# Kernel optimization log

Measured on AMD Instinct MI355X. Metric: run time of the kernel, lower is better.

The kernel has to match this reference:

```python
import jax, jax.numpy as jnp
import numpy as np

# ADMM hyperparameters for mode='only_tv'
GAMMA_TV = 10.0
ALPHA = 5.0
LAMBDA_TV = 1e-4
N_ITERS = 50


def soft_thresh(v, t):
    return jnp.sign(v) * jnp.maximum(jnp.abs(v) - t, 0.0)


def setup_inputs() -> dict:
    key = jax.random.key(0)
    k1, k2, k3 = jax.random.split(key, 3)
    target = jax.random.normal(k1, (4096,), dtype=jnp.float32)
    A = jax.random.normal(k2, (9, 4096), dtype=jnp.float32)  # [M, N], post-transpose
    x0 = jax.random.normal(k3, (4096,), dtype=jnp.float32)   # replaces torch.randn_like
    return {"target": target, "A": A, "x0": x0}


def reference(target, A, x0):
    N = A.shape[1]
    I = jnp.eye(N, dtype=A.dtype)
    Delta = jnp.roll(I, 1, axis=1) - I               # [N, N] circular difference
    DtD = Delta.T @ Delta
    AtA = A.T @ A
    # only_tv: gamma_l1 = beta = 0, so regularizer is ATA + gamma_tv*DtD + alpha*I
    inv_item = jnp.linalg.inv(AtA + GAMMA_TV * DtD + ALPHA * I)

    b = A @ target            # [M]
    bA = b @ A                # [N], constant across iterations

    def step(carry, _):
        x, eta_tv, tau = carry
        # u_tv: soft-threshold of backward difference (roll along axis 0)
        u_tv = soft_thresh(jnp.roll(x, 1, axis=0) - x + eta_tv / GAMMA_TV,
                           LAMBDA_TV / GAMMA_TV)
        # w: nonnegativity split variable
        w = jnp.maximum(x + tau / ALPHA, 0.0)
        # x-update (zero terms for l1/dwt/z dropped: gamma_l1 = gamma_dwt = beta = 0)
        resid = bA + (GAMMA_TV * u_tv - eta_tv) + (ALPHA * w - tau)
        x = resid @ inv_item
        # dual updates
        eta_tv = eta_tv + GAMMA_TV * (Delta @ x - u_tv)
        tau = tau + ALPHA * (x - w)
        return (x, eta_tv, tau), None

    zeros = jnp.zeros_like(x0)
    (x, _, _), _ = jax.lax.scan(step, (x0, zeros, zeros), None, length=N_ITERS)
    return x
```

## Files before the change

### kernel.cpp

```cpp
#include <hip/hip_runtime.h>
#include <math.h>

#define NT 512
#define EPT 8
#define NN 4096
#define MM 9
#define NIT 50

#define LAM  3.90625e-3f
#define LAM2 1.52587890625e-5f
#define K1LAST 0.3333282470703125f

template<int CTRL, int RMASK>
__device__ __forceinline__ float dpp_add(float v) {
  int m = __builtin_amdgcn_update_dpp(0, __builtin_bit_cast(int, v), CTRL, RMASK, 0xf, false);
  return v + __builtin_bit_cast(float, m);
}
__device__ __forceinline__ float wave_sum(float v) {
  v = dpp_add<0x111, 0xf>(v);
  v = dpp_add<0x112, 0xf>(v);
  v = dpp_add<0x114, 0xf>(v);
  v = dpp_add<0x118, 0xf>(v);
  v = dpp_add<0x142, 0xa>(v);
  v = dpp_add<0x143, 0xc>(v);
  return v;
}
template<int CTRL>
__device__ __forceinline__ float dpp_shift(float oldv, float v) {
  int m = __builtin_amdgcn_update_dpp(__builtin_bit_cast(int, oldv),
                                      __builtin_bit_cast(int, v), CTRL, 0xf, 0xf, false);
  return __builtin_bit_cast(float, m);
}
__device__ __forceinline__ float bcast_lane(float v, int l) {
  return __builtin_bit_cast(float, __builtin_amdgcn_readlane(__builtin_bit_cast(int, v), l));
}

__device__ __forceinline__ void solveM_pre(const float r[EPT], float pl0[EPT],
                                           float2* __restrict__ s_sc, int t) {
  float yl[EPT];
  yl[EPT - 1] = r[EPT - 1] * 0.1f;
#pragma unroll
  for (int j = EPT - 2; j >= 0; --j) yl[j] = fmaf(0.5f, yl[j + 1], r[j] * 0.1f);
  pl0[0] = 0.5f * yl[0];
#pragma unroll
  for (int j = 1; j < EPT; ++j) pl0[j] = 0.5f * (yl[j] + pl0[j - 1]);
  s_sc[t] = make_float2(yl[0], pl0[EPT - 1]);
}

__device__ __forceinline__ void solveM_post(const float pl0[EPT], float p[EPT],
                                            const float2* __restrict__ s_sc, int t) {
  const float K1[EPT] = {0.001953125f, 0.0048828125f, 0.01025390625f, 0.020751953125f,
                         0.0416259765625f, 0.08331298828125f, 0.166656494140625f,
                         0.3333282470703125f};
  float2 g[7];
#pragma unroll
  for (int k = 0; k < 7; ++k) g[k] = s_sc[(t + k - 3) & (NT - 1)];
  float c  = fmaf(LAM2, g[6].x, fmaf(LAM, g[5].x, g[4].x));
  float s1 = fmaf(LAM2, g[0].y, fmaf(LAM, g[1].y, g[2].y));
  float s2 = g[3].x;
  s2 = fmaf(LAM, g[2].x + g[4].x, s2);
  s2 = fmaf(LAM2, g[1].x + g[5].x, s2);
  float c2 = fmaf(K1LAST, s2, s1);
  float f2 = 0.5f;
#pragma unroll
  for (int j = 0; j < EPT; ++j) {
    p[j] = fmaf(c2, f2, fmaf(c, K1[j], pl0[j]));
    f2 *= 0.5f;
  }
}

__global__ void __launch_bounds__(NT, 2)
admm_kernel(const float* __restrict__ tg, const float* __restrict__ Ag,
            const float* __restrict__ x0, float* __restrict__ out) {
  __shared__ float2 s_sc[NT];
  __shared__ __align__(16) float s_wq[8][12];
  __shared__ float s_S[MM * MM];
  __shared__ float s_L[MM * MM];
  __shared__ float s_edge[8][2];

  const int t = threadIdx.x;
  const int base = t * EPT;
  const int lane = t & 63, wave = t >> 6;

  float A[MM][EPT];
#pragma unroll
  for (int m = 0; m < MM; ++m) {
    float4 a0 = *(const float4*)(Ag + m * NN + base);
    float4 a1 = *(const float4*)(Ag + m * NN + base + 4);
    A[m][0] = a0.x; A[m][1] = a0.y; A[m][2] = a0.z; A[m][3] = a0.w;
    A[m][4] = a1.x; A[m][5] = a1.y; A[m][6] = a1.z; A[m][7] = a1.w;
  }

  float x[EPT], tgt[EPT];
  {
    float4 v0 = *(const float4*)(x0 + base);
    float4 v1 = *(const float4*)(x0 + base + 4);
    x[0] = v0.x; x[1] = v0.y; x[2] = v0.z; x[3] = v0.w;
    x[4] = v1.x; x[5] = v1.y; x[6] = v1.z; x[7] = v1.w;
    float4 t0 = *(const float4*)(tg + base);
    float4 t1 = *(const float4*)(tg + base + 4);
    tgt[0] = t0.x; tgt[1] = t0.y; tgt[2] = t0.z; tgt[3] = t0.w;
    tgt[4] = t1.x; tgt[5] = t1.y; tgt[6] = t1.z; tgt[7] = t1.w;
  }
  if (lane == 0)  s_edge[wave][0] = x[0];
  if (lane == 63) s_edge[wave][1] = x[7];

  float pq[MM];
#pragma unroll
  for (int m = 0; m < MM; ++m) {
    float s = 0.f;
#pragma unroll
    for (int j = 0; j < EPT; ++j) s = fmaf(A[m][j], tgt[j], s);
    pq[m] = wave_sum(s);
  }
  if (lane == 63) {
    *(float4*)&s_wq[wave][0] = make_float4(pq[0], pq[1], pq[2], pq[3]);
    *(float4*)&s_wq[wave][4] = make_float4(pq[4], pq[5], pq[6], pq[7]);
    s_wq[wave][8] = pq[8];
  }
  __syncthreads();
  float bb[MM];
  {
    float zv = 0.f;
    if (lane < MM) {
#pragma unroll
      for (int wv = 0; wv < 8; ++wv) zv += s_wq[wv][lane];
    }
#pragma unroll
    for (int m = 0; m < MM; ++m) bb[m] = bcast_lane(zv, m);
  }
  float bA[EPT];
#pragma unroll
  for (int j = 0; j < EPT; ++j) {
    float s = 0.f;
#pragma unroll
    for (int m = 0; m < MM; ++m) s = fmaf(bb[m], A[m][j], s);
    bA[j] = s;
  }

  float G[MM][EPT];
#pragma unroll
  for (int mc = 0; mc < MM; ++mc) {
    float rin[EPT];
#pragma unroll
    for (int j = 0; j < EPT; ++j) rin[j] = A[mc][j];
    float pl0[EPT];
    solveM_pre(rin, pl0, s_sc, t);
    __syncthreads();
    float gcol[EPT];
    solveM_post(pl0, gcol, s_sc, t);
#pragma unroll
    for (int j = 0; j < EPT; ++j) G[mc][j] = gcol[j];
#pragma unroll
    for (int k = 0; k < MM; ++k) {
      float s = 0.f;
#pragma unroll
      for (int j = 0; j < EPT; ++j) s = fmaf(A[k][j], gcol[j], s);
      pq[k] = wave_sum(s);
    }
    if (lane == 63) {
      *(float4*)&s_wq[wave][0] = make_float4(pq[0], pq[1], pq[2], pq[3]);
      *(float4*)&s_wq[wave][4] = make_float4(pq[4], pq[5], pq[6], pq[7]);
      s_wq[wave][8] = pq[8];
    }
    __syncthreads();
    if (wave == 0 && lane < MM) {
      float s = 0.f;
#pragma unroll
      for (int wv = 0; wv < 8; ++wv) s += s_wq[wv][lane];
      s_S[lane * MM + mc] = s + ((lane == mc) ? 1.f : 0.f);
    }
  }

  if (t < 64) {
    float row[2 * MM];
#pragma unroll
    for (int j = 0; j < MM; ++j) row[j] = (t < MM) ? s_S[t * MM + j] : 0.f;
#pragma unroll
    for (int j = 0; j < MM; ++j) row[MM + j] = (j == t) ? 1.f : 0.f;
#pragma unroll
    for (int pp = 0; pp < MM; ++pp) {
      float pr[2 * MM];
#pragma unroll
      for (int j = 0; j < 2 * MM; ++j) pr[j] = __shfl(row[j], pp, 64);
      float rpiv = 1.f / pr[pp];
      float fct = row[pp] * rpiv;
#pragma unroll
      for (int j = 0; j < 2 * MM; ++j)
        row[j] = (t == pp) ? pr[j] * rpiv : fmaf(-fct, pr[j], row[j]);
    }
    float crow[MM];
#pragma unroll
    for (int j = 0; j < MM; ++j) crow[j] = row[MM + j];
#pragma unroll
    for (int k = 0; k < MM; ++k) {
      float dk = __shfl(crow[k], k, 64);
      float inv = 1.f / sqrtf(dk);
      crow[k] *= inv;
#pragma unroll
      for (int jj = k + 1; jj < MM; ++jj) {
        float ljk = __shfl(crow[k], jj, 64);
        crow[jj] = fmaf(-crow[k], ljk, crow[jj]);
      }
    }
    if (t < MM) {
#pragma unroll
      for (int j = 0; j < MM; ++j) s_L[t * MM + j] = (t >= j) ? crow[j] : 0.f;
    }
  }
  __syncthreads();

  float GH[MM][EPT];
#pragma unroll
  for (int m = 0; m < MM; ++m) {
    float lcol[MM];
#pragma unroll
    for (int k = 0; k < MM; ++k) lcol[k] = s_L[k * MM + m];
#pragma unroll
    for (int j = 0; j < EPT; ++j) {
      float s = 0.f;
#pragma unroll
      for (int k = 0; k < MM; ++k)
        if (k >= m) s = fmaf(G[k][j], lcol[k], s);
      GH[m][j] = s;
    }
  }

  float eta[EPT], tau[EPT];
#pragma unroll
  for (int j = 0; j < EPT; ++j) { eta[j] = 0.f; tau[j] = 0.f; }
  float u7prev = 0.f, w7prev = 0.f;

#pragma unroll 1
  for (int it = 0; it < NIT; ++it) {
    float oldm = 0.f, oldn = 0.f;
    if (lane == 0)  oldm = s_edge[(wave + 7) & 7][1];
    if (lane == 63) oldn = s_edge[(wave + 1) & 7][0];
    float xm1 = dpp_shift<0x138>(oldm, x[7]);
    if (it) {
      float xn8 = dpp_shift<0x130>(oldn, x[0]);
      eta[7] = fmaf(10.f, (xn8 - x[7]) - u7prev, eta[7]);
      tau[7] = fmaf(5.f, x[7] - w7prev, tau[7]);
    }
    float u[EPT], w[EPT], r[EPT];
#pragma unroll
    for (int j = 0; j < EPT; ++j) {
      float xprev = (j == 0) ? xm1 : x[j - 1];
      float v = xprev - x[j] + eta[j] * 0.1f;
      u[j] = copysignf(fmaxf(fabsf(v) - 1e-5f, 0.f), v);
      w[j] = fmaxf(fmaf(tau[j], 0.2f, x[j]), 0.f);
      r[j] = bA[j] + 10.f * u[j] - eta[j] + 5.f * w[j] - tau[j];
    }
    float zp[MM];
#pragma unroll
    for (int m = 0; m < MM; ++m) {
      float s = 0.f;
#pragma unroll
      for (int j = 0; j < EPT; ++j) s = fmaf(GH[m][j], r[j], s);
      zp[m] = wave_sum(s);
    }
    if (lane == 63) {
      *(float4*)&s_wq[wave][0] = make_float4(zp[0], zp[1], zp[2], zp[3]);
      *(float4*)&s_wq[wave][4] = make_float4(zp[4], zp[5], zp[6], zp[7]);
      s_wq[wave][8] = zp[8];
    }
    float pl0[EPT];
    solveM_pre(r, pl0, s_sc, t);
    __syncthreads();
    float p[EPT];
    solveM_post(pl0, p, s_sc, t);
    float zv = 0.f;
    if (lane < MM) {
#pragma unroll
      for (int wv = 0; wv < 8; ++wv) zv += s_wq[wv][lane];
    }
    float z[MM];
#pragma unroll
    for (int m = 0; m < MM; ++m) z[m] = bcast_lane(zv, m);
#pragma unroll
    for (int j = 0; j < EPT; ++j) {
      float s = p[j];
#pragma unroll
      for (int m = 0; m < MM; ++m) s = fmaf(-GH[m][j], z[m], s);
      x[j] = s;
    }
    if (lane == 0)  s_edge[wave][0] = x[0];
    if (lane == 63) s_edge[wave][1] = x[7];
#pragma unroll
    for (int j = 0; j < EPT - 1; ++j) {
      eta[j] = fmaf(10.f, (x[j + 1] - x[j]) - u[j], eta[j]);
      tau[j] = fmaf(5.f, x[j] - w[j], tau[j]);
    }
    u7prev = u[7]; w7prev = w[7];
    __syncthreads();
  }

  float4 o0, o1;
  o0.x = x[0]; o0.y = x[1]; o0.z = x[2]; o0.w = x[3];
  o1.x = x[4]; o1.y = x[5]; o1.z = x[6]; o1.w = x[7];
  *(float4*)(out + base) = o0;
  *(float4*)(out + base + 4) = o1;
}

extern "C" void kernel_launch(void* const* d_in, const int* in_sizes, int n_in,
                              void* d_out, int out_size, void* d_ws, size_t ws_size,
                              hipStream_t stream) {
  const float* target = (const float*)d_in[0];
  const float* A      = (const float*)d_in[1];
  const float* x0     = (const float*)d_in[2];
  admm_kernel<<<1, NT, 0, stream>>>(target, A, x0, (float*)d_out);
}
```

Measured before the change: 106.5 us.

## Cut to one barrier per ADMM iteration by recomputing neighbor x values and double buffering

The main loop is restructured so each iteration has a single __syncthreads instead of two. Neighbor boundary values x[-1] and x[8] are no longer exchanged through shared memory. They are recomputed locally from a wider 9-entry gather of scan carries plus neighbor GH rows kept in shared memory. The scan and reduction buffers are double-buffered by iteration parity, and the first iteration's residual is peeled before the loop. This trades extra FMAs and shared-memory loads per iteration for one fewer block-wide barrier on the serial critical path.

```diff
diff --git a/kernel.cpp b/kernel.cpp
--- a/kernel.cpp
+++ b/kernel.cpp
@@ -10,6 +10,7 @@
 #define LAM  3.90625e-3f
 #define LAM2 1.52587890625e-5f
 #define K1LAST 0.3333282470703125f
+#define HALF8 3.90625e-3f
 
 template<int CTRL, int RMASK>
 __device__ __forceinline__ float dpp_add(float v) {
@@ -25,12 +26,6 @@
   v = dpp_add<0x143, 0xc>(v);
   return v;
 }
-template<int CTRL>
-__device__ __forceinline__ float dpp_shift(float oldv, float v) {
-  int m = __builtin_amdgcn_update_dpp(__builtin_bit_cast(int, oldv),
-                                      __builtin_bit_cast(int, v), CTRL, 0xf, 0xf, false);
-  return __builtin_bit_cast(float, m);
-}
 __device__ __forceinline__ float bcast_lane(float v, int l) {
   return __builtin_bit_cast(float, __builtin_amdgcn_readlane(__builtin_bit_cast(int, v), l));
 }
@@ -47,36 +42,63 @@
   s_sc[t] = make_float2(yl[0], pl0[EPT - 1]);
 }
 
-__device__ __forceinline__ void solveM_post(const float pl0[EPT], float p[EPT],
-                                            const float2* __restrict__ s_sc, int t) {
+__device__ __forceinline__ void gather9(const float2* __restrict__ s_sc, int t, float2 g[9]) {
+#pragma unroll
+  for (int k = 0; k < 9; ++k) g[k] = s_sc[(t + k - 4) & (NT - 1)];
+}
+
+__device__ __forceinline__ void carries_own(const float2 g[9], float& c, float& c2) {
+  c = fmaf(LAM2, g[7].x, fmaf(LAM, g[6].x, g[5].x));
+  float s1 = fmaf(LAM2, g[1].y, fmaf(LAM, g[2].y, g[3].y));
+  float s2 = g[4].x;
+  s2 = fmaf(LAM, g[3].x + g[5].x, s2);
+  s2 = fmaf(LAM2, g[2].x + g[6].x, s2);
+  c2 = fmaf(K1LAST, s2, s1);
+}
+
+__device__ __forceinline__ void finish_own(const float2 g[9], const float pl0[EPT], float p[EPT]) {
   const float K1[EPT] = {0.001953125f, 0.0048828125f, 0.01025390625f, 0.020751953125f,
                          0.0416259765625f, 0.08331298828125f, 0.166656494140625f,
-                         0.3333282470703125f};
-  float2 g[7];
-#pragma unroll
-  for (int k = 0; k < 7; ++k) g[k] = s_sc[(t + k - 3) & (NT - 1)];
-  float c  = fmaf(LAM2, g[6].x, fmaf(LAM, g[5].x, g[4].x));
+                         K1LAST};
+  float c, c2;
+  carries_own(g, c, c2);
+  float f2 = 0.5f;
+#pragma unroll
+  for (int j = 0; j < EPT; ++j) {
+    p[j] = fmaf(c2, f2, fmaf(c, K1[j], pl0[j]));
+    f2 *= 0.5f;
+  }
+}
+
+__device__ __forceinline__ float p7_prev(const float2 g[9]) {
+  float c = fmaf(LAM2, g[6].x, fmaf(LAM, g[5].x, g[4].x));
   float s1 = fmaf(LAM2, g[0].y, fmaf(LAM, g[1].y, g[2].y));
   float s2 = g[3].x;
   s2 = fmaf(LAM, g[2].x + g[4].x, s2);
   s2 = fmaf(LAM2, g[1].x + g[5].x, s2);
   float c2 = fmaf(K1LAST, s2, s1);
-  float f2 = 0.5f;
-#pragma unroll
-  for (int j = 0; j < EPT; ++j) {
-    p[j] = fmaf(c2, f2, fmaf(c, K1[j], pl0[j]));
-    f2 *= 0.5f;
-  }
+  return fmaf(c2, HALF8, fmaf(c, K1LAST, g[3].y));
+}
+
+__device__ __forceinline__ float p0_next(const float2 g[9]) {
+  float c = fmaf(LAM2, g[8].x, fmaf(LAM, g[7].x, g[6].x));
+  float s1 = fmaf(LAM2, g[2].y, fmaf(LAM, g[3].y, g[4].y));
+  float s2 = g[5].x;
+  s2 = fmaf(LAM, g[4].x + g[6].x, s2);
+  s2 = fmaf(LAM2, g[3].x + g[7].x, s2);
+  float c2 = fmaf(K1LAST, s2, s1);
+  return fmaf(c2, 0.5f, fmaf(c, 0.001953125f, 0.5f * g[5].x));
 }
 
 __global__ void __launch_bounds__(NT, 2)
 admm_kernel(const float* __restrict__ tg, const float* __restrict__ Ag,
             const float* __restrict__ x0, float* __restrict__ out) {
-  __shared__ float2 s_sc[NT];
-  __shared__ __align__(16) float s_wq[8][12];
+  __shared__ float2 s_sc[2][NT];
+  __shared__ __align__(16) float s_wq[2][8][12];
   __shared__ float s_S[MM * MM];
   __shared__ float s_L[MM * MM];
-  __shared__ float s_edge[8][2];
+  __shared__ float s_gh7[NT][MM];
+  __shared__ float s_gh0[NT][MM];
 
   const int t = threadIdx.x;
   const int base = t * EPT;
@@ -102,8 +124,7 @@
     tgt[0] = t0.x; tgt[1] = t0.y; tgt[2] = t0.z; tgt[3] = t0.w;
     tgt[4] = t1.x; tgt[5] = t1.y; tgt[6] = t1.z; tgt[7] = t1.w;
   }
-  if (lane == 0)  s_edge[wave][0] = x[0];
-  if (lane == 63) s_edge[wave][1] = x[7];
+  float xm1_0 = x0[(base + NN - 1) & (NN - 1)];
 
   float pq[MM];
 #pragma unroll
@@ -114,9 +135,9 @@
     pq[m] = wave_sum(s);
   }
   if (lane == 63) {
-    *(float4*)&s_wq[wave][0] = make_float4(pq[0], pq[1], pq[2], pq[3]);
-    *(float4*)&s_wq[wave][4] = make_float4(pq[4], pq[5], pq[6], pq[7]);
-    s_wq[wave][8] = pq[8];
+    *(float4*)&s_wq[0][wave][0] = make_float4(pq[0], pq[1], pq[2], pq[3]);
+    *(float4*)&s_wq[0][wave][4] = make_float4(pq[4], pq[5], pq[6], pq[7]);
+    s_wq[0][wave][8] = pq[8];
   }
   __syncthreads();
   float bb[MM];
@@ -124,7 +145,7 @@
     float zv = 0.f;
     if (lane < MM) {
 #pragma unroll
-      for (int wv = 0; wv < 8; ++wv) zv += s_wq[wv][lane];
+      for (int wv = 0; wv < 8; ++wv) zv += s_wq[0][wv][lane];
     }
 #pragma unroll
     for (int m = 0; m < MM; ++m) bb[m] = bcast_lane(zv, m);
@@ -145,10 +166,12 @@
 #pragma unroll
     for (int j = 0; j < EPT; ++j) rin[j] = A[mc][j];
     float pl0[EPT];
-    solveM_pre(rin, pl0, s_sc, t);
+    solveM_pre(rin, pl0, &s_sc[mc & 1][0], t);
     __syncthreads();
+    float2 g[9];
+    gather9(&s_sc[mc & 1][0], t, g);
     float gcol[EPT];
-    solveM_post(pl0, gcol, s_sc, t);
+    finish_own(g, pl0, gcol);
 #pragma unroll
     for (int j = 0; j < EPT; ++j) G[mc][j] = gcol[j];
 #pragma unroll
@@ -159,15 +182,15 @@
       pq[k] = wave_sum(s);
     }
     if (lane == 63) {
-      *(float4*)&s_wq[wave][0] = make_float4(pq[0], pq[1], pq[2], pq[3]);
-      *(float4*)&s_wq[wave][4] = make_float4(pq[4], pq[5], pq[6], pq[7]);
-      s_wq[wave][8] = pq[8];
+      *(float4*)&s_wq[0][wave][0] = make_float4(pq[0], pq[1], pq[2], pq[3]);
+      *(float4*)&s_wq[0][wave][4] = make_float4(pq[4], pq[5], pq[6], pq[7]);
+      s_wq[0][wave][8] = pq[8];
     }
     __syncthreads();
     if (wave == 0 && lane < MM) {
       float s = 0.f;
 #pragma unroll
-      for (int wv = 0; wv < 8; ++wv) s += s_wq[wv][lane];
+      for (int wv = 0; wv < 8; ++wv) s += s_wq[0][wv][lane];
       s_S[lane * MM + mc] = s + ((lane == mc) ? 1.f : 0.f);
     }
   }
@@ -225,24 +248,84 @@
       GH[m][j] = s;
     }
   }
+#pragma unroll
+  for (int m = 0; m < MM; ++m) {
+    s_gh7[t][m] = GH[m][7];
+    s_gh0[t][m] = GH[m][0];
+  }
 
   float eta[EPT], tau[EPT];
 #pragma unroll
   for (int j = 0; j < EPT; ++j) { eta[j] = 0.f; tau[j] = 0.f; }
-  float u7prev = 0.f, w7prev = 0.f;
+  float u[EPT], w[EPT], r[EPT], pl0[EPT];
+#pragma unroll
+  for (int j = 0; j < EPT; ++j) {
+    float xprev = (j == 0) ? xm1_0 : x[j - 1];
+    float v = xprev - x[j];
+    u[j] = copysignf(fmaxf(fabsf(v) - 1e-5f, 0.f), v);
+    w[j] = fmaxf(x[j], 0.f);
+    r[j] = bA[j] + 10.f * u[j] + 5.f * w[j];
+  }
+  {
+    float zp[MM];
+#pragma unroll
+    for (int m = 0; m < MM; ++m) {
+      float s = 0.f;
+#pragma unroll
+      for (int j = 0; j < EPT; ++j) s = fmaf(GH[m][j], r[j], s);
+      zp[m] = wave_sum(s);
+    }
+    if (lane == 63) {
+      *(float4*)&s_wq[0][wave][0] = make_float4(zp[0], zp[1], zp[2], zp[3]);
+      *(float4*)&s_wq[0][wave][4] = make_float4(zp[4], zp[5], zp[6], zp[7]);
+      s_wq[0][wave][8] = zp[8];
+    }
+  }
+  solveM_pre(r, pl0, &s_sc[0][0], t);
+  __syncthreads();
 
 #pragma unroll 1
   for (int it = 0; it < NIT; ++it) {
-    float oldm = 0.f, oldn = 0.f;
-    if (lane == 0)  oldm = s_edge[(wave + 7) & 7][1];
-    if (lane == 63) oldn = s_edge[(wave + 1) & 7][0];
-    float xm1 = dpp_shift<0x138>(oldm, x[7]);
-    if (it) {
-      float xn8 = dpp_shift<0x130>(oldn, x[0]);
-      eta[7] = fmaf(10.f, (xn8 - x[7]) - u7prev, eta[7]);
-      tau[7] = fmaf(5.f, x[7] - w7prev, tau[7]);
-    }
-    float u[EPT], w[EPT], r[EPT];
+    const int rp = it & 1;
+    float2 g[9];
+    gather9(&s_sc[rp][0], t, g);
+    float gh7r[MM], gh0r[MM];
+    {
+      const int tm = (t + NT - 1) & (NT - 1), tp = (t + 1) & (NT - 1);
+#pragma unroll
+      for (int m = 0; m < MM; ++m) { gh7r[m] = s_gh7[tm][m]; gh0r[m] = s_gh0[tp][m]; }
+    }
+    float zv = 0.f;
+    if (lane < MM) {
+#pragma unroll
+      for (int wv = 0; wv < 8; ++wv) zv += s_wq[rp][wv][lane];
+    }
+    float z[MM];
+#pragma unroll
+    for (int m = 0; m < MM; ++m) z[m] = bcast_lane(zv, m);
+    float p[EPT];
+    finish_own(g, pl0, p);
+#pragma unroll
+    for (int j = 0; j < EPT; ++j) {
+      float s = p[j];
+#pragma unroll
+      for (int m = 0; m < MM; ++m) s = fmaf(-GH[m][j], z[m], s);
+      x[j] = s;
+    }
+    if (it == NIT - 1) break;
+    float xm1 = p7_prev(g);
+#pragma unroll
+    for (int m = 0; m < MM; ++m) xm1 = fmaf(-gh7r[m], z[m], xm1);
+    float xp1 = p0_next(g);
+#pragma unroll
+    for (int m = 0; m < MM; ++m) xp1 = fmaf(-gh0r[m], z[m], xp1);
+#pragma unroll
+    for (int j = 0; j < EPT - 1; ++j) {
+      eta[j] = fmaf(10.f, (x[j + 1] - x[j]) - u[j], eta[j]);
+      tau[j] = fmaf(5.f, x[j] - w[j], tau[j]);
+    }
+    eta[7] = fmaf(10.f, (xp1 - x[7]) - u[7], eta[7]);
+    tau[7] = fmaf(5.f, x[7] - w[7], tau[7]);
 #pragma unroll
     for (int j = 0; j < EPT; ++j) {
       float xprev = (j == 0) ? xm1 : x[j - 1];
@@ -260,38 +343,11 @@
       zp[m] = wave_sum(s);
     }
     if (lane == 63) {
-      *(float4*)&s_wq[wave][0] = make_float4(zp[0], zp[1], zp[2], zp[3]);
-      *(float4*)&s_wq[wave][4] = make_float4(zp[4], zp[5], zp[6], zp[7]);
-      s_wq[wave][8] = zp[8];
-    }
-    float pl0[EPT];
-    solveM_pre(r, pl0, s_sc, t);
-    __syncthreads();
-    float p[EPT];
-    solveM_post(pl0, p, s_sc, t);
-    float zv = 0.f;
-    if (lane < MM) {
-#pragma unroll
-      for (int wv = 0; wv < 8; ++wv) zv += s_wq[wv][lane];
-    }
-    float z[MM];
-#pragma unroll
-    for (int m = 0; m < MM; ++m) z[m] = bcast_lane(zv, m);
-#pragma unroll
-    for (int j = 0; j < EPT; ++j) {
-      float s = p[j];
-#pragma unroll
-      for (int m = 0; m < MM; ++m) s = fmaf(-GH[m][j], z[m], s);
-      x[j] = s;
-    }
-    if (lane == 0)  s_edge[wave][0] = x[0];
-    if (lane == 63) s_edge[wave][1] = x[7];
-#pragma unroll
-    for (int j = 0; j < EPT - 1; ++j) {
-      eta[j] = fmaf(10.f, (x[j + 1] - x[j]) - u[j], eta[j]);
-      tau[j] = fmaf(5.f, x[j] - w[j], tau[j]);
-    }
-    u7prev = u[7]; w7prev = w[7];
+      *(float4*)&s_wq[rp ^ 1][wave][0] = make_float4(zp[0], zp[1], zp[2], zp[3]);
+      *(float4*)&s_wq[rp ^ 1][wave][4] = make_float4(zp[4], zp[5], zp[6], zp[7]);
+      s_wq[rp ^ 1][wave][8] = zp[8];
+    }
+    solveM_pre(r, pl0, &s_sc[rp ^ 1][0], t);
     __syncthreads();
   }
 
```

New measurement: 114.1 us. +7.1%, slower.

## Double threads to 1024 with 4 elements each and rescale ADMM dual variables

Applied to the files above, without the earlier changes.

Launches 1024 threads with 4 elements each instead of 512 with 8, so there are 16 waves and the per-thread serial work and register use are halved. The tridiagonal-like solve now gathers 11 neighbour partials with new decay constants, and the Gram-column setup alternates between two shared scratch buffers. The dual variables are kept pre-scaled (eta/10, tau/5) and the nonnegativity split is rewritten as max(x, -tau5), which removes several multiplies per element. In exchange, the cross-wave reductions now sum over 16 wave partials, the barrier spans more waves, and each solve reads more shared memory.

```diff
diff --git a/kernel.cpp b/kernel.cpp
--- a/kernel.cpp
+++ b/kernel.cpp
@@ -1,15 +1,16 @@
 #include <hip/hip_runtime.h>
 #include <math.h>
 
-#define NT 512
-#define EPT 8
+#define NT 1024
+#define EPT 4
+#define NW (NT/64)
 #define NN 4096
 #define MM 9
 #define NIT 50
 
-#define LAM  3.90625e-3f
-#define LAM2 1.52587890625e-5f
-#define K1LAST 0.3333282470703125f
+#define LAM  0.0625f
+#define LAM2 3.90625e-3f
+#define K1L  0.33203125f
 
 template<int CTRL, int RMASK>
 __device__ __forceinline__ float dpp_add(float v) {
@@ -38,45 +39,42 @@
 __device__ __forceinline__ void solveM_pre(const float r[EPT], float pl0[EPT],
                                            float2* __restrict__ s_sc, int t) {
   float yl[EPT];
-  yl[EPT - 1] = r[EPT - 1] * 0.1f;
-#pragma unroll
-  for (int j = EPT - 2; j >= 0; --j) yl[j] = fmaf(0.5f, yl[j + 1], r[j] * 0.1f);
+  yl[3] = r[3] * 0.1f;
+  yl[2] = fmaf(0.5f, yl[3], r[2] * 0.1f);
+  yl[1] = fmaf(0.5f, yl[2], r[1] * 0.1f);
+  yl[0] = fmaf(0.5f, yl[1], r[0] * 0.1f);
   pl0[0] = 0.5f * yl[0];
-#pragma unroll
-  for (int j = 1; j < EPT; ++j) pl0[j] = 0.5f * (yl[j] + pl0[j - 1]);
-  s_sc[t] = make_float2(yl[0], pl0[EPT - 1]);
-}
-
-__device__ __forceinline__ void solveM_post(const float pl0[EPT], float p[EPT],
-                                            const float2* __restrict__ s_sc, int t) {
-  const float K1[EPT] = {0.001953125f, 0.0048828125f, 0.01025390625f, 0.020751953125f,
-                         0.0416259765625f, 0.08331298828125f, 0.166656494140625f,
-                         0.3333282470703125f};
-  float2 g[7];
-#pragma unroll
-  for (int k = 0; k < 7; ++k) g[k] = s_sc[(t + k - 3) & (NT - 1)];
-  float c  = fmaf(LAM2, g[6].x, fmaf(LAM, g[5].x, g[4].x));
-  float s1 = fmaf(LAM2, g[0].y, fmaf(LAM, g[1].y, g[2].y));
-  float s2 = g[3].x;
-  s2 = fmaf(LAM, g[2].x + g[4].x, s2);
-  s2 = fmaf(LAM2, g[1].x + g[5].x, s2);
-  float c2 = fmaf(K1LAST, s2, s1);
-  float f2 = 0.5f;
-#pragma unroll
-  for (int j = 0; j < EPT; ++j) {
-    p[j] = fmaf(c2, f2, fmaf(c, K1[j], pl0[j]));
-    f2 *= 0.5f;
-  }
-}
-
-__global__ void __launch_bounds__(NT, 2)
+  pl0[1] = 0.5f * (yl[1] + pl0[0]);
+  pl0[2] = 0.5f * (yl[2] + pl0[1]);
+  pl0[3] = 0.5f * (yl[3] + pl0[2]);
+  s_sc[t] = make_float2(yl[0], pl0[3]);
+}
+
+__device__ __forceinline__ void gather11(const float2* __restrict__ s_sc, int t, float2 g[11]) {
+#pragma unroll
+  for (int k = 0; k < 11; ++k) g[k] = s_sc[(t + k - 5) & (NT - 1)];
+}
+
+__device__ __forceinline__ void finish_own(const float2 g[11], const float pl0[EPT], float p[EPT]) {
+  float c = fmaf(LAM, fmaf(LAM, fmaf(LAM, fmaf(LAM, g[10].x, g[9].x), g[8].x), g[7].x), g[6].x);
+  float s1 = fmaf(LAM, fmaf(LAM, fmaf(LAM, fmaf(LAM, g[0].y, g[1].y), g[2].y), g[3].y), g[4].y);
+  float s2 = fmaf(LAM, fmaf(LAM, fmaf(LAM, fmaf(LAM, g[1].x + g[9].x, g[2].x + g[8].x),
+                                      g[3].x + g[7].x), g[4].x + g[6].x), g[5].x);
+  float c2 = fmaf(1.0f / 3.0f, s2, s1);
+  p[0] = fmaf(c2, 0.5f,    fmaf(c, 0.03125f,   pl0[0]));
+  p[1] = fmaf(c2, 0.25f,   fmaf(c, 0.078125f,  pl0[1]));
+  p[2] = fmaf(c2, 0.125f,  fmaf(c, 0.1640625f, pl0[2]));
+  p[3] = fmaf(c2, 0.0625f, fmaf(c, K1L,        pl0[3]));
+}
+
+__global__ void __launch_bounds__(NT, 4)
 admm_kernel(const float* __restrict__ tg, const float* __restrict__ Ag,
             const float* __restrict__ x0, float* __restrict__ out) {
-  __shared__ float2 s_sc[NT];
-  __shared__ __align__(16) float s_wq[8][12];
+  __shared__ float2 s_sc[2][NT];
+  __shared__ __align__(16) float s_wq[NW][12];
   __shared__ float s_S[MM * MM];
   __shared__ float s_L[MM * MM];
-  __shared__ float s_edge[8][2];
+  __shared__ float s_edge[NW][2];
 
   const int t = threadIdx.x;
   const int base = t * EPT;
@@ -86,24 +84,18 @@
 #pragma unroll
   for (int m = 0; m < MM; ++m) {
     float4 a0 = *(const float4*)(Ag + m * NN + base);
-    float4 a1 = *(const float4*)(Ag + m * NN + base + 4);
     A[m][0] = a0.x; A[m][1] = a0.y; A[m][2] = a0.z; A[m][3] = a0.w;
-    A[m][4] = a1.x; A[m][5] = a1.y; A[m][6] = a1.z; A[m][7] = a1.w;
   }
 
   float x[EPT], tgt[EPT];
   {
     float4 v0 = *(const float4*)(x0 + base);
-    float4 v1 = *(const float4*)(x0 + base + 4);
     x[0] = v0.x; x[1] = v0.y; x[2] = v0.z; x[3] = v0.w;
-    x[4] = v1.x; x[5] = v1.y; x[6] = v1.z; x[7] = v1.w;
     float4 t0 = *(const float4*)(tg + base);
-    float4 t1 = *(const float4*)(tg + base + 4);
     tgt[0] = t0.x; tgt[1] = t0.y; tgt[2] = t0.z; tgt[3] = t0.w;
-    tgt[4] = t1.x; tgt[5] = t1.y; tgt[6] = t1.z; tgt[7] = t1.w;
   }
   if (lane == 0)  s_edge[wave][0] = x[0];
-  if (lane == 63) s_edge[wave][1] = x[7];
+  if (lane == 63) s_edge[wave][1] = x[3];
 
   float pq[MM];
 #pragma unroll
@@ -124,7 +116,7 @@
     float zv = 0.f;
     if (lane < MM) {
 #pragma unroll
-      for (int wv = 0; wv < 8; ++wv) zv += s_wq[wv][lane];
+      for (int wv = 0; wv < NW; ++wv) zv += s_wq[wv][lane];
     }
 #pragma unroll
     for (int m = 0; m < MM; ++m) bb[m] = bcast_lane(zv, m);
@@ -145,10 +137,12 @@
 #pragma unroll
     for (int j = 0; j < EPT; ++j) rin[j] = A[mc][j];
     float pl0[EPT];
-    solveM_pre(rin, pl0, s_sc, t);
+    solveM_pre(rin, pl0, &s_sc[mc & 1][0], t);
     __syncthreads();
+    float2 g[11];
+    gather11(&s_sc[mc & 1][0], t, g);
     float gcol[EPT];
-    solveM_post(pl0, gcol, s_sc, t);
+    finish_own(g, pl0, gcol);
 #pragma unroll
     for (int j = 0; j < EPT; ++j) G[mc][j] = gcol[j];
 #pragma unroll
@@ -167,7 +161,7 @@
     if (wave == 0 && lane < MM) {
       float s = 0.f;
 #pragma unroll
-      for (int wv = 0; wv < 8; ++wv) s += s_wq[wv][lane];
+      for (int wv = 0; wv < NW; ++wv) s += s_wq[wv][lane];
       s_S[lane * MM + mc] = s + ((lane == mc) ? 1.f : 0.f);
     }
   }
@@ -226,30 +220,29 @@
     }
   }
 
-  float eta[EPT], tau[EPT];
-#pragma unroll
-  for (int j = 0; j < EPT; ++j) { eta[j] = 0.f; tau[j] = 0.f; }
-  float u7prev = 0.f, w7prev = 0.f;
+  float eta10[EPT], tau5[EPT];
+#pragma unroll
+  for (int j = 0; j < EPT; ++j) { eta10[j] = 0.f; tau5[j] = 0.f; }
+  float u3prev = 0.f;
 
 #pragma unroll 1
   for (int it = 0; it < NIT; ++it) {
     float oldm = 0.f, oldn = 0.f;
-    if (lane == 0)  oldm = s_edge[(wave + 7) & 7][1];
-    if (lane == 63) oldn = s_edge[(wave + 1) & 7][0];
-    float xm1 = dpp_shift<0x138>(oldm, x[7]);
+    if (lane == 0)  oldm = s_edge[(wave + NW - 1) & (NW - 1)][1];
+    if (lane == 63) oldn = s_edge[(wave + 1) & (NW - 1)][0];
+    float xm1 = dpp_shift<0x138>(oldm, x[3]);
     if (it) {
-      float xn8 = dpp_shift<0x130>(oldn, x[0]);
-      eta[7] = fmaf(10.f, (xn8 - x[7]) - u7prev, eta[7]);
-      tau[7] = fmaf(5.f, x[7] - w7prev, tau[7]);
-    }
-    float u[EPT], w[EPT], r[EPT];
+      float xn4 = dpp_shift<0x130>(oldn, x[0]);
+      eta10[3] += (xn4 - x[3]) - u3prev;
+    }
+    float u[EPT], m1a[EPT], r[EPT];
 #pragma unroll
     for (int j = 0; j < EPT; ++j) {
       float xprev = (j == 0) ? xm1 : x[j - 1];
-      float v = xprev - x[j] + eta[j] * 0.1f;
+      float v = xprev - x[j] + eta10[j];
       u[j] = copysignf(fmaxf(fabsf(v) - 1e-5f, 0.f), v);
-      w[j] = fmaxf(fmaf(tau[j], 0.2f, x[j]), 0.f);
-      r[j] = bA[j] + 10.f * u[j] - eta[j] + 5.f * w[j] - tau[j];
+      m1a[j] = fmaxf(x[j], -tau5[j]);
+      r[j] = fmaf(10.f, u[j] - eta10[j], fmaf(5.f, m1a[j], bA[j]));
     }
     float zp[MM];
 #pragma unroll
@@ -265,14 +258,16 @@
       s_wq[wave][8] = zp[8];
     }
     float pl0[EPT];
-    solveM_pre(r, pl0, s_sc, t);
+    solveM_pre(r, pl0, &s_sc[0][0], t);
     __syncthreads();
+    float2 g[11];
+    gather11(&s_sc[0][0], t, g);
     float p[EPT];
-    solveM_post(pl0, p, s_sc, t);
+    finish_own(g, pl0, p);
     float zv = 0.f;
     if (lane < MM) {
 #pragma unroll
-      for (int wv = 0; wv < 8; ++wv) zv += s_wq[wv][lane];
+      for (int wv = 0; wv < NW; ++wv) zv += s_wq[wv][lane];
     }
     float z[MM];
 #pragma unroll
@@ -285,21 +280,20 @@
       x[j] = s;
     }
     if (lane == 0)  s_edge[wave][0] = x[0];
-    if (lane == 63) s_edge[wave][1] = x[7];
-#pragma unroll
-    for (int j = 0; j < EPT - 1; ++j) {
-      eta[j] = fmaf(10.f, (x[j + 1] - x[j]) - u[j], eta[j]);
-      tau[j] = fmaf(5.f, x[j] - w[j], tau[j]);
-    }
-    u7prev = u[7]; w7prev = w[7];
+    if (lane == 63) s_edge[wave][1] = x[3];
+#pragma unroll
+    for (int j = 0; j < EPT - 1; ++j)
+      eta10[j] += (x[j + 1] - x[j]) - u[j];
+#pragma unroll
+    for (int j = 0; j < EPT; ++j)
+      tau5[j] = x[j] - m1a[j];
+    u3prev = u[3];
     __syncthreads();
   }
 
-  float4 o0, o1;
+  float4 o0;
   o0.x = x[0]; o0.y = x[1]; o0.z = x[2]; o0.w = x[3];
-  o1.x = x[4]; o1.y = x[5]; o1.z = x[6]; o1.w = x[7];
   *(float4*)(out + base) = o0;
-  *(float4*)(out + base + 4) = o1;
 }
 
 extern "C" void kernel_launch(void* const* d_in, const int* in_sizes, int n_in,
```

New measurement: 145.1 us. 36.3% more time.

## Pack ADMM iteration math into v_pk_fma and rescale dual variables

Applied to the files above, without the earlier changes.

Stores x, GH and the reduction inputs as float2 pairs and uses inline v_pk_fma_f32/v_pk_mul_f32 for the GH·r reductions and the x reconstruction. The dual variables are rescaled so eta is kept divided by gamma and tau is stored as an offset, which removes several multiplies per element. The preprocessing scratch buffer is also double-buffered across the column solves. This cuts VALU instruction count in the serial 50-iteration loop of a single-block kernel, at the cost of hand-written asm that constrains register allocation and packing moves.

```diff
diff --git a/kernel.cpp b/kernel.cpp
--- a/kernel.cpp
+++ b/kernel.cpp
@@ -10,6 +10,16 @@
 #define LAM  3.90625e-3f
 #define LAM2 1.52587890625e-5f
 #define K1LAST 0.3333282470703125f
+
+typedef float f2 __attribute__((ext_vector_type(2)));
+__device__ __forceinline__ f2 mkf2(float a, float b) { f2 v; v.x = a; v.y = b; return v; }
+
+__device__ __forceinline__ f2 pkfma(f2 a, f2 b, f2 c) {
+  f2 d; asm("v_pk_fma_f32 %0, %1, %2, %3" : "=v"(d) : "v"(a), "v"(b), "v"(c)); return d;
+}
+__device__ __forceinline__ f2 pkmul(f2 a, f2 b) {
+  f2 d; asm("v_pk_mul_f32 %0, %1, %2" : "=v"(d) : "v"(a), "v"(b)); return d;
+}
 
 template<int CTRL, int RMASK>
 __device__ __forceinline__ float dpp_add(float v) {
@@ -51,7 +61,7 @@
                                             const float2* __restrict__ s_sc, int t) {
   const float K1[EPT] = {0.001953125f, 0.0048828125f, 0.01025390625f, 0.020751953125f,
                          0.0416259765625f, 0.08331298828125f, 0.166656494140625f,
-                         0.3333282470703125f};
+                         K1LAST};
   float2 g[7];
 #pragma unroll
   for (int k = 0; k < 7; ++k) g[k] = s_sc[(t + k - 3) & (NT - 1)];
@@ -61,18 +71,18 @@
   s2 = fmaf(LAM, g[2].x + g[4].x, s2);
   s2 = fmaf(LAM2, g[1].x + g[5].x, s2);
   float c2 = fmaf(K1LAST, s2, s1);
-  float f2 = 0.5f;
+  float f2w = 0.5f;
 #pragma unroll
   for (int j = 0; j < EPT; ++j) {
-    p[j] = fmaf(c2, f2, fmaf(c, K1[j], pl0[j]));
-    f2 *= 0.5f;
+    p[j] = fmaf(c2, f2w, fmaf(c, K1[j], pl0[j]));
+    f2w *= 0.5f;
   }
 }
 
 __global__ void __launch_bounds__(NT, 2)
 admm_kernel(const float* __restrict__ tg, const float* __restrict__ Ag,
             const float* __restrict__ x0, float* __restrict__ out) {
-  __shared__ float2 s_sc[NT];
+  __shared__ float2 s_sc[2][NT];
   __shared__ __align__(16) float s_wq[8][12];
   __shared__ float s_S[MM * MM];
   __shared__ float s_L[MM * MM];
@@ -129,13 +139,16 @@
 #pragma unroll
     for (int m = 0; m < MM; ++m) bb[m] = bcast_lane(zv, m);
   }
-  float bA[EPT];
-#pragma unroll
-  for (int j = 0; j < EPT; ++j) {
-    float s = 0.f;
-#pragma unroll
-    for (int m = 0; m < MM; ++m) s = fmaf(bb[m], A[m][j], s);
-    bA[j] = s;
+  f2 bA2[4];
+#pragma unroll
+  for (int jj = 0; jj < 4; ++jj) {
+    float sa = 0.f, sb = 0.f;
+#pragma unroll
+    for (int m = 0; m < MM; ++m) {
+      sa = fmaf(bb[m], A[m][2 * jj], sa);
+      sb = fmaf(bb[m], A[m][2 * jj + 1], sb);
+    }
+    bA2[jj] = mkf2(sa, sb);
   }
 
   float G[MM][EPT];
@@ -145,10 +158,10 @@
 #pragma unroll
     for (int j = 0; j < EPT; ++j) rin[j] = A[mc][j];
     float pl0[EPT];
-    solveM_pre(rin, pl0, s_sc, t);
+    solveM_pre(rin, pl0, (float2*)&s_sc[mc & 1][0], t);
     __syncthreads();
     float gcol[EPT];
-    solveM_post(pl0, gcol, s_sc, t);
+    solveM_post(pl0, gcol, (const float2*)&s_sc[mc & 1][0], t);
 #pragma unroll
     for (int j = 0; j < EPT; ++j) G[mc][j] = gcol[j];
 #pragma unroll
@@ -210,54 +223,71 @@
   }
   __syncthreads();
 
-  float GH[MM][EPT];
+  f2 GH2[MM][4];
 #pragma unroll
   for (int m = 0; m < MM; ++m) {
     float lcol[MM];
 #pragma unroll
     for (int k = 0; k < MM; ++k) lcol[k] = s_L[k * MM + m];
 #pragma unroll
-    for (int j = 0; j < EPT; ++j) {
-      float s = 0.f;
+    for (int jj = 0; jj < 4; ++jj) {
+      float sa = 0.f, sb = 0.f;
 #pragma unroll
       for (int k = 0; k < MM; ++k)
-        if (k >= m) s = fmaf(G[k][j], lcol[k], s);
-      GH[m][j] = s;
-    }
-  }
-
-  float eta[EPT], tau[EPT];
-#pragma unroll
-  for (int j = 0; j < EPT; ++j) { eta[j] = 0.f; tau[j] = 0.f; }
-  float u7prev = 0.f, w7prev = 0.f;
+        if (k >= m) {
+          sa = fmaf(G[k][2 * jj], lcol[k], sa);
+          sb = fmaf(G[k][2 * jj + 1], lcol[k], sb);
+        }
+      GH2[m][jj] = mkf2(sa, sb);
+    }
+  }
+
+  f2 x2[4], eta2[4], tau2[4];
+#pragma unroll
+  for (int jj = 0; jj < 4; ++jj) {
+    x2[jj] = mkf2(x[2 * jj], x[2 * jj + 1]);
+    eta2[jj] = mkf2(0.f, 0.f);
+    tau2[jj] = mkf2(0.f, 0.f);
+  }
+  float u7prev = 0.f;
 
 #pragma unroll 1
   for (int it = 0; it < NIT; ++it) {
     float oldm = 0.f, oldn = 0.f;
     if (lane == 0)  oldm = s_edge[(wave + 7) & 7][1];
     if (lane == 63) oldn = s_edge[(wave + 1) & 7][0];
-    float xm1 = dpp_shift<0x138>(oldm, x[7]);
+    float xm1 = dpp_shift<0x138>(oldm, x2[3].y);
     if (it) {
-      float xn8 = dpp_shift<0x130>(oldn, x[0]);
-      eta[7] = fmaf(10.f, (xn8 - x[7]) - u7prev, eta[7]);
-      tau[7] = fmaf(5.f, x[7] - w7prev, tau[7]);
-    }
-    float u[EPT], w[EPT], r[EPT];
-#pragma unroll
-    for (int j = 0; j < EPT; ++j) {
-      float xprev = (j == 0) ? xm1 : x[j - 1];
-      float v = xprev - x[j] + eta[j] * 0.1f;
-      u[j] = copysignf(fmaxf(fabsf(v) - 1e-5f, 0.f), v);
-      w[j] = fmaxf(fmaf(tau[j], 0.2f, x[j]), 0.f);
-      r[j] = bA[j] + 10.f * u[j] - eta[j] + 5.f * w[j] - tau[j];
+      float xn8 = dpp_shift<0x130>(oldn, x2[0].x);
+      eta2[3].y += (xn8 - x2[3].y) - u7prev;
+    }
+    float u[EPT], m1[EPT], rr[EPT];
+    f2 r2[4];
+#pragma unroll
+    for (int jj = 0; jj < 4; ++jj) {
+      float xa = x2[jj].x, xb = x2[jj].y;
+      float xprev = (jj == 0) ? xm1 : x2[jj - 1].y;
+      float va = xprev - xa + eta2[jj].x;
+      float vb = xa - xb + eta2[jj].y;
+      float ua = copysignf(fmaxf(fabsf(va) - 1e-5f, 0.f), va);
+      float ub = copysignf(fmaxf(fabsf(vb) - 1e-5f, 0.f), vb);
+      float ma = fmaxf(xa, -tau2[jj].x);
+      float mb = fmaxf(xb, -tau2[jj].y);
+      float ra = fmaf(10.f, ua - eta2[jj].x, fmaf(5.f, ma, bA2[jj].x));
+      float rb = fmaf(10.f, ub - eta2[jj].y, fmaf(5.f, mb, bA2[jj].y));
+      u[2 * jj] = ua; u[2 * jj + 1] = ub;
+      m1[2 * jj] = ma; m1[2 * jj + 1] = mb;
+      rr[2 * jj] = ra; rr[2 * jj + 1] = rb;
+      r2[jj] = mkf2(ra, rb);
     }
     float zp[MM];
 #pragma unroll
     for (int m = 0; m < MM; ++m) {
-      float s = 0.f;
-#pragma unroll
-      for (int j = 0; j < EPT; ++j) s = fmaf(GH[m][j], r[j], s);
-      zp[m] = wave_sum(s);
+      f2 acc = pkmul(GH2[m][0], r2[0]);
+      acc = pkfma(GH2[m][1], r2[1], acc);
+      acc = pkfma(GH2[m][2], r2[2], acc);
+      acc = pkfma(GH2[m][3], r2[3], acc);
+      zp[m] = wave_sum(acc.x + acc.y);
     }
     if (lane == 63) {
       *(float4*)&s_wq[wave][0] = make_float4(zp[0], zp[1], zp[2], zp[3]);
@@ -265,39 +295,44 @@
       s_wq[wave][8] = zp[8];
     }
     float pl0[EPT];
-    solveM_pre(r, pl0, s_sc, t);
+    solveM_pre(rr, pl0, (float2*)&s_sc[0][0], t);
     __syncthreads();
     float p[EPT];
-    solveM_post(pl0, p, s_sc, t);
+    solveM_post(pl0, p, (const float2*)&s_sc[0][0], t);
     float zv = 0.f;
     if (lane < MM) {
 #pragma unroll
       for (int wv = 0; wv < 8; ++wv) zv += s_wq[wv][lane];
     }
-    float z[MM];
-#pragma unroll
-    for (int m = 0; m < MM; ++m) z[m] = bcast_lane(zv, m);
-#pragma unroll
-    for (int j = 0; j < EPT; ++j) {
-      float s = p[j];
-#pragma unroll
-      for (int m = 0; m < MM; ++m) s = fmaf(-GH[m][j], z[m], s);
-      x[j] = s;
-    }
-    if (lane == 0)  s_edge[wave][0] = x[0];
-    if (lane == 63) s_edge[wave][1] = x[7];
-#pragma unroll
-    for (int j = 0; j < EPT - 1; ++j) {
-      eta[j] = fmaf(10.f, (x[j + 1] - x[j]) - u[j], eta[j]);
-      tau[j] = fmaf(5.f, x[j] - w[j], tau[j]);
-    }
-    u7prev = u[7]; w7prev = w[7];
+    f2 zn2[MM];
+#pragma unroll
+    for (int m = 0; m < MM; ++m) {
+      float zn = -bcast_lane(zv, m);
+      zn2[m] = mkf2(zn, zn);
+    }
+#pragma unroll
+    for (int jj = 0; jj < 4; ++jj) {
+      f2 acc = mkf2(p[2 * jj], p[2 * jj + 1]);
+#pragma unroll
+      for (int m = 0; m < MM; ++m) acc = pkfma(GH2[m][jj], zn2[m], acc);
+      x2[jj] = acc;
+    }
+    if (lane == 0)  s_edge[wave][0] = x2[0].x;
+    if (lane == 63) s_edge[wave][1] = x2[3].y;
+#pragma unroll
+    for (int jj = 0; jj < 4; ++jj) {
+      float xa = x2[jj].x, xb = x2[jj].y;
+      eta2[jj].x += (xb - xa) - u[2 * jj];
+      if (jj < 3) eta2[jj].y += (x2[jj + 1].x - xb) - u[2 * jj + 1];
+      tau2[jj] = mkf2(xa - m1[2 * jj], xb - m1[2 * jj + 1]);
+    }
+    u7prev = u[7];
     __syncthreads();
   }
 
   float4 o0, o1;
-  o0.x = x[0]; o0.y = x[1]; o0.z = x[2]; o0.w = x[3];
-  o1.x = x[4]; o1.y = x[5]; o1.z = x[6]; o1.w = x[7];
+  o0.x = x2[0].x; o0.y = x2[0].y; o0.z = x2[1].x; o0.w = x2[1].y;
+  o1.x = x2[2].x; o1.y = x2[2].y; o1.z = x2[3].x; o1.w = x2[3].y;
   *(float4*)(out + base) = o0;
   *(float4*)(out + base + 4) = o1;
 }
```

Result: slower. 109.7 us (+3.0%).
